# Kernel tuning notes

Measured on AMD Instinct MI355X. Metric: run time of the kernel, lower is better.

The kernel has to match this reference:

```python
import jax, jax.numpy as jnp
import numpy as np

B, S, H, NH, I, V, P, T = 8, 512, 768, 12, 3072, 30522, 512, 2
D = H // NH
EPS = 1e-12


def _ln(x, g, b):
    m = x.mean(-1, keepdims=True)
    v = ((x - m) ** 2).mean(-1, keepdims=True)
    return (x - m) / jnp.sqrt(v + EPS) * g + b


def setup_inputs() -> dict:
    key = jax.random.key(0)
    ks = jax.random.split(key, 24)
    s = 0.02
    f32 = jnp.float32
    d = {
        'x': jax.random.randint(ks[0], (B, S), 0, V, dtype=jnp.int32),
        'W_word': (jax.random.normal(ks[1], (V, H)) * s).astype(f32),
        'W_pos': (jax.random.normal(ks[2], (P, H)) * s).astype(f32),
        'W_type': (jax.random.normal(ks[3], (T, H)) * s).astype(f32),
        'g_emb': jnp.ones((H,), f32), 'b_emb': jnp.zeros((H,), f32),
        'Wq': (jax.random.normal(ks[4], (H, H)) * s).astype(f32), 'bq': jnp.zeros((H,), f32),
        'Wk': (jax.random.normal(ks[5], (H, H)) * s).astype(f32), 'bk': jnp.zeros((H,), f32),
        'Wv': (jax.random.normal(ks[6], (H, H)) * s).astype(f32), 'bv': jnp.zeros((H,), f32),
        'Wo': (jax.random.normal(ks[7], (H, H)) * s).astype(f32), 'bo': jnp.zeros((H,), f32),
        'g_attn': jnp.ones((H,), f32), 'b_attn': jnp.zeros((H,), f32),
        'Wi': (jax.random.normal(ks[8], (H, I)) * s).astype(f32), 'bi': jnp.zeros((I,), f32),
        'Wd': (jax.random.normal(ks[9], (I, H)) * s).astype(f32), 'bd': jnp.zeros((H,), f32),
        'g_out': jnp.ones((H,), f32), 'b_out': jnp.zeros((H,), f32),
        'Wp': (jax.random.normal(ks[10], (H, H)) * s).astype(f32), 'bp': jnp.zeros((H,), f32),
    }
    return d


def _forward(x, W_word, W_pos, W_type, g_emb, b_emb, Wq, bq, Wk, bk, Wv, bv,
             Wo, bo, g_attn, b_attn, Wi, bi, Wd, bd, g_out, b_out, Wp, bp):
    # embeddings: word + position(arange) + token_type(all zeros -> row 0)
    h = W_word[x] + W_pos[jnp.arange(S)][None, :, :] + W_type[0][None, None, :]
    h = _ln(h, g_emb, b_emb)
    scale = 1.0 / jnp.sqrt(jnp.float32(D))
    # NOTE: the torch module shares one set of layer weights across all 6 layers.
    for _ in range(6):
        q = (h @ Wq + bq).reshape(B, S, NH, D).transpose(0, 2, 1, 3)  # bhsd
        k = (h @ Wk + bk).reshape(B, S, NH, D).transpose(0, 2, 1, 3)
        v = (h @ Wv + bv).reshape(B, S, NH, D).transpose(0, 2, 1, 3)
        scores = jnp.einsum('bhqd,bhkd->bhqk', q, k) * scale
        probs = jax.nn.softmax(scores, axis=-1)
        ctx = jnp.einsum('bhqk,bhkd->bhqd', probs, v)
        ctx = ctx.transpose(0, 2, 1, 3).reshape(B, S, H)
        attn = ctx @ Wo + bo
        xa = _ln(h + attn, g_attn, b_attn)
        ff = jax.nn.gelu(xa @ Wi + bi, approximate=False) @ Wd + bd
        h = _ln(xa + ff, g_out, b_out)
    pooled = h[:, 0, :] @ Wp + bp  # no tanh in the original module
    return h, pooled


def reference(x, W_word, W_pos, W_type, g_emb, b_emb, Wq, bq, Wk, bk, Wv, bv,
              Wo, bo, g_attn, b_attn, Wi, bi, Wd, bd, g_out, b_out, Wp, bp):
    return _forward(x, W_word, W_pos, W_type, g_emb, b_emb, Wq, bq, Wk, bk, Wv, bv,
                    Wo, bo, g_attn, b_attn, Wi, bi, Wd, bd, g_out, b_out, Wp, bp)
```

## Files before the change

### kernel.cpp

```cpp
#include <hip/hip_runtime.h>
#include <hip/hip_bf16.h>
#include <math.h>

#define B_  8
#define S_  512
#define H_  768
#define NH_ 12
#define D_  64
#define I_  3072
#define NTOK (B_*S_)
#define LDQ 2304

typedef __attribute__((ext_vector_type(8))) __bf16 bf16x8;
typedef __attribute__((ext_vector_type(8))) unsigned short ushort8;
typedef __attribute__((ext_vector_type(4))) float  f32x4;

__device__ __forceinline__ float gelu_exact(float x) {
    return 0.5f * x * (1.0f + erff(x * 0.70710678118654752440f));
}

__device__ __forceinline__ unsigned short f2bf(float x) {
    __hip_bfloat16 h = __float2bfloat16(x);
    return *reinterpret_cast<unsigned short*>(&h);
}

__device__ __forceinline__ void gload16(const void* g, void* l) {
    __builtin_amdgcn_global_load_lds(
        (const __attribute__((address_space(1))) void*)g,
        (__attribute__((address_space(3))) void*)l,
        16, 0, 0);
}

#define SB0() __builtin_amdgcn_sched_barrier(0)

__global__ void cvtT_kernel(const float* __restrict__ W, __hip_bfloat16* __restrict__ WT,
                            int K, int N) {
    __shared__ float tile[32][33];
    int k0 = blockIdx.y * 32, n0 = blockIdx.x * 32;
    int tx = threadIdx.x & 31, ty = threadIdx.x >> 5;
    #pragma unroll
    for (int i = 0; i < 32; i += 8)
        tile[ty + i][tx] = W[(long)(k0 + ty + i) * N + n0 + tx];
    __syncthreads();
    #pragma unroll
    for (int i = 0; i < 32; i += 8)
        WT[(long)(n0 + ty + i) * K + k0 + tx] = __float2bfloat16(tile[tx][ty + i]);
}

__global__ void embed_ln_kernel(const int* __restrict__ ids,
                                const float* __restrict__ Wword,
                                const float* __restrict__ Wpos,
                                const float* __restrict__ Wtype,
                                const float* __restrict__ g,
                                const float* __restrict__ b,
                                float* __restrict__ out,
                                __hip_bfloat16* __restrict__ outb) {
    int t = blockIdx.x;
    int s = t % S_;
    long id = ids[t];
    int tid = threadIdx.x;
    float vals[3];
    float sum = 0.f, sq = 0.f;
    #pragma unroll
    for (int i = 0; i < 3; ++i) {
        int c = tid + 256 * i;
        float e = Wword[id * H_ + c] + Wpos[(long)s * H_ + c] + Wtype[c];
        vals[i] = e; sum += e; sq += e * e;
    }
    __shared__ float r1[256], r2[256];
    r1[tid] = sum; r2[tid] = sq; __syncthreads();
    for (int st = 128; st > 0; st >>= 1) {
        if (tid < st) { r1[tid] += r1[tid + st]; r2[tid] += r2[tid + st]; }
        __syncthreads();
    }
    float mean = r1[0] * (1.0f / H_);
    float var  = r2[0] * (1.0f / H_) - mean * mean;
    float inv  = rsqrtf(var + 1e-12f);
    #pragma unroll
    for (int i = 0; i < 3; ++i) {
        int c = tid + 256 * i;
        float v = (vals[i] - mean) * inv * g[c] + b[c];
        out[(long)t * H_ + c] = v;
        outb[(long)t * H_ + c] = __float2bfloat16(v);
    }
}

__global__ void add_ln_kernel(const float* __restrict__ a,
                              const float* __restrict__ r,
                              const float* __restrict__ g,
                              const float* __restrict__ bb,
                              float* __restrict__ out,
                              __hip_bfloat16* __restrict__ outb) {
    int t = blockIdx.x;
    int tid = threadIdx.x;
    float vals[3];
    float sum = 0.f, sq = 0.f;
    #pragma unroll
    for (int i = 0; i < 3; ++i) {
        int c = tid + 256 * i;
        float e = a[(long)t * H_ + c] + r[(long)t * H_ + c];
        vals[i] = e; sum += e; sq += e * e;
    }
    __shared__ float r1[256], r2[256];
    r1[tid] = sum; r2[tid] = sq; __syncthreads();
    for (int st = 128; st > 0; st >>= 1) {
        if (tid < st) { r1[tid] += r1[tid + st]; r2[tid] += r2[tid + st]; }
        __syncthreads();
    }
    float mean = r1[0] * (1.0f / H_);
    float var  = r2[0] * (1.0f / H_) - mean * mean;
    float inv  = rsqrtf(var + 1e-12f);
    #pragma unroll
    for (int i = 0; i < 3; ++i) {
        int c = tid + 256 * i;
        float v = (vals[i] - mean) * inv * g[c] + bb[c];
        out[(long)t * H_ + c] = v;
        outb[(long)t * H_ + c] = __float2bfloat16(v);
    }
}

__global__ void add_ln3_kernel(const float* __restrict__ a,
                               const float* __restrict__ r1p,
                               const float* __restrict__ r2p,
                               const float* __restrict__ g,
                               const float* __restrict__ bb,
                               float* __restrict__ out,
                               __hip_bfloat16* __restrict__ outb) {
    int t = blockIdx.x;
    int tid = threadIdx.x;
    float vals[3];
    float sum = 0.f, sq = 0.f;
    #pragma unroll
    for (int i = 0; i < 3; ++i) {
        int c = tid + 256 * i;
        float e = a[(long)t * H_ + c] + r1p[(long)t * H_ + c] + r2p[(long)t * H_ + c];
        vals[i] = e; sum += e; sq += e * e;
    }
    __shared__ float r1[256], r2[256];
    r1[tid] = sum; r2[tid] = sq; __syncthreads();
    for (int st = 128; st > 0; st >>= 1) {
        if (tid < st) { r1[tid] += r1[tid + st]; r2[tid] += r2[tid + st]; }
        __syncthreads();
    }
    float mean = r1[0] * (1.0f / H_);
    float var  = r2[0] * (1.0f / H_) - mean * mean;
    float inv  = rsqrtf(var + 1e-12f);
    #pragma unroll
    for (int i = 0; i < 3; ++i) {
        int c = tid + 256 * i;
        float v = (vals[i] - mean) * inv * g[c] + bb[c];
        out[(long)t * H_ + c] = v;
        outb[(long)t * H_ + c] = __float2bfloat16(v);
    }
}

template<int BM, int BN, int MI, int NJ, int ACT, int WF32, int WB16>
__global__ __launch_bounds__(256, 6) void mfma_gemm_kernel(
    const __hip_bfloat16* __restrict__ A,
    const __hip_bfloat16* __restrict__ BT,
    const float* __restrict__ bias,
    float* __restrict__ Cf,
    __hip_bfloat16* __restrict__ Cb,
    int M, int N, int Kc, int lda, int ldb) {
    constexpr int WC = BN / (NJ * 16);
    constexpr int WR = BM / (MI * 16);
    static_assert(WR * WC == 4, "4 waves");
    constexpr int LA = BM * 4 / 256;
    constexpr int LB = BN * 4 / 256;
    constexpr int L  = LA + LB;
    __shared__ __align__(16) __hip_bfloat16 sA[2][BM * 32];
    __shared__ __align__(16) __hip_bfloat16 sB[2][BN * 32];
    const int tid  = threadIdx.x;
    const int lane = tid & 63;
    const int w    = tid >> 6;
    const int wr   = w / WC, wc = w % WC;
    const int l15  = lane & 15, l4 = lane >> 4;
    const int m0 = blockIdx.y * BM, n0 = blockIdx.x * BN;
    const int koff = blockIdx.z * Kc;
    const int goff = (l15 >> 1) & 3;

    auto stage = [&](int buf, int k0) {
        #pragma unroll
        for (int t = 0; t < LA; ++t) {
            int c = tid + 256 * t;
            int row = c >> 2, gq = c & 3;
            int gsrc = gq ^ ((row >> 1) & 3);
            gload16(A + (long)(m0 + row) * lda + koff + k0 + gsrc * 8, &sA[buf][row * 32 + gq * 8]);
        }
        #pragma unroll
        for (int t = 0; t < LB; ++t) {
            int c = tid + 256 * t;
            int row = c >> 2, gq = c & 3;
            int gsrc = gq ^ ((row >> 1) & 3);
            gload16(BT + (long)(n0 + row) * ldb + koff + k0 + gsrc * 8, &sB[buf][row * 32 + gq * 8]);
        }
    };

    f32x4 acc[MI][NJ] = {};
    const int nk = Kc >> 5;

    stage(0, 0);
    for (int t = 0; t < nk; ++t) {
        const int cur = t & 1;
        if (t + 1 < nk) {
            stage(cur ^ 1, (t + 1) * 32);
            asm volatile("s_waitcnt vmcnt(%0)" :: "i"(L) : "memory");
        } else {
            asm volatile("s_waitcnt vmcnt(0)" ::: "memory");
        }
        SB0(); __builtin_amdgcn_s_barrier(); SB0();

        const int gsw = (l4 ^ goff) * 8;
        bf16x8 af[MI], bf[NJ];
        #pragma unroll
        for (int i = 0; i < MI; ++i)
            af[i] = *reinterpret_cast<const bf16x8*>(&sA[cur][(wr * MI * 16 + i * 16 + l15) * 32 + gsw]);
        #pragma unroll
        for (int j = 0; j < NJ; ++j)
            bf[j] = *reinterpret_cast<const bf16x8*>(&sB[cur][(wc * NJ * 16 + j * 16 + l15) * 32 + gsw]);
        #pragma unroll
        for (int i = 0; i < MI; ++i)
            #pragma unroll
            for (int j = 0; j < NJ; ++j)
                acc[i][j] = __builtin_amdgcn_mfma_f32_16x16x32_bf16(af[i], bf[j], acc[i][j], 0, 0, 0);

        SB0(); __builtin_amdgcn_s_barrier(); SB0();
    }

    float* Cfz = Cf + (size_t)blockIdx.z * M * N;
    const bool addb = (blockIdx.z == 0);
    #pragma unroll
    for (int i = 0; i < MI; ++i) {
        #pragma unroll
        for (int j = 0; j < NJ; ++j) {
            int col = n0 + wc * NJ * 16 + j * 16 + l15;
            float bv = addb ? bias[col] : 0.f;
            #pragma unroll
            for (int r = 0; r < 4; ++r) {
                int row = m0 + wr * MI * 16 + i * 16 + l4 * 4 + r;
                float v = acc[i][j][r] + bv;
                if (ACT == 1) v = gelu_exact(v);
                if (WF32) Cfz[(long)row * N + col] = v;
                if (WB16) Cb[(long)row * N + col] = __float2bfloat16(v);
            }
        }
    }
}

__global__ __launch_bounds__(256, 4) void flash_attn_kernel(
    const __hip_bfloat16* __restrict__ QKV,
    __hip_bfloat16* __restrict__ Ctx) {
    __shared__ __align__(16) unsigned short sK[64 * 72];
    __shared__ __align__(16) unsigned short sVt[64 * 72];
    __shared__ __align__(16) unsigned short sP[4 * 16 * 72];

    const int tid  = threadIdx.x;
    const int lane = tid & 63;
    const int w    = tid >> 6;
    const int l15  = lane & 15, l4 = lane >> 4;
    const int qb = blockIdx.x;
    const int bh = blockIdx.y;
    const int b  = bh / NH_, hd = bh % NH_;
    const long rbase = (long)b * S_ * LDQ;
    const int qoff = hd * D_, koff = H_ + hd * D_, voff = 2 * H_ + hd * D_;

    const int qrow0 = qb * 64 + w * 16;
    bf16x8 af[2];
    #pragma unroll
    for (int ks = 0; ks < 2; ++ks)
        af[ks] = *reinterpret_cast<const bf16x8*>(
            QKV + rbase + (long)(qrow0 + l15) * LDQ + qoff + ks * 32 + l4 * 8);

    f32x4 ctx[4] = {};
    float m_run[4], l_run[4];
    #pragma unroll
    for (int r = 0; r < 4; ++r) { m_run[r] = -1e30f; l_run[r] = 0.f; }

    const int sr = tid >> 2;
    const int sc = (tid & 3) * 16;
    unsigned short* pl = sP + w * (16 * 72);

    for (int kv0 = 0; kv0 < S_; kv0 += 64) {
        const __hip_bfloat16* kg = QKV + rbase + (long)(kv0 + sr) * LDQ + koff + sc;
        const __hip_bfloat16* vg = QKV + rbase + (long)(kv0 + sr) * LDQ + voff + sc;
        ushort8 kv_a = *reinterpret_cast<const ushort8*>(kg);
        ushort8 kv_b = *reinterpret_cast<const ushort8*>(kg + 8);
        ushort8 vv_a = *reinterpret_cast<const ushort8*>(vg);
        ushort8 vv_b = *reinterpret_cast<const ushort8*>(vg + 8);
        __syncthreads();
        *reinterpret_cast<ushort8*>(sK + sr * 72 + sc)     = kv_a;
        *reinterpret_cast<ushort8*>(sK + sr * 72 + sc + 8) = kv_b;
        #pragma unroll
        for (int i = 0; i < 8; ++i) {
            sVt[(sc + i) * 72 + sr]     = vv_a[i];
            sVt[(sc + 8 + i) * 72 + sr] = vv_b[i];
        }
        __syncthreads();

        f32x4 s[4];
        #pragma unroll
        for (int j = 0; j < 4; ++j) {
            s[j] = (f32x4){0.f, 0.f, 0.f, 0.f};
            #pragma unroll
            for (int ks = 0; ks < 2; ++ks) {
                bf16x8 bk = *reinterpret_cast<const bf16x8*>(sK + (j * 16 + l15) * 72 + ks * 32 + l4 * 8);
                s[j] = __builtin_amdgcn_mfma_f32_16x16x32_bf16(af[ks], bk, s[j], 0, 0, 0);
            }
        }
        #pragma unroll
        for (int j = 0; j < 4; ++j) s[j] *= 0.125f;

        #pragma unroll
        for (int r = 0; r < 4; ++r) {
            float mx = fmaxf(fmaxf(s[0][r], s[1][r]), fmaxf(s[2][r], s[3][r]));
            #pragma unroll
            for (int o = 1; o < 16; o <<= 1) mx = fmaxf(mx, __shfl_xor(mx, o));
            float mnew = fmaxf(m_run[r], mx);
            float sum = 0.f;
            #pragma unroll
            for (int j = 0; j < 4; ++j) {
                float p = __expf(s[j][r] - mnew);
                s[j][r] = p; sum += p;
            }
            #pragma unroll
            for (int o = 1; o < 16; o <<= 1) sum += __shfl_xor(sum, o);
            float resc = __expf(m_run[r] - mnew);
            l_run[r] = l_run[r] * resc + sum;
            m_run[r] = mnew;
            #pragma unroll
            for (int j = 0; j < 4; ++j) ctx[j][r] *= resc;
        }

        #pragma unroll
        for (int j = 0; j < 4; ++j)
            #pragma unroll
            for (int r = 0; r < 4; ++r)
                pl[(l4 * 4 + r) * 72 + j * 16 + l15] = f2bf(s[j][r]);

        #pragma unroll
        for (int ks = 0; ks < 2; ++ks) {
            bf16x8 ap = *reinterpret_cast<const bf16x8*>(pl + l15 * 72 + ks * 32 + l4 * 8);
            #pragma unroll
            for (int jd = 0; jd < 4; ++jd) {
                bf16x8 bv = *reinterpret_cast<const bf16x8*>(sVt + (jd * 16 + l15) * 72 + ks * 32 + l4 * 8);
                ctx[jd] = __builtin_amdgcn_mfma_f32_16x16x32_bf16(ap, bv, ctx[jd], 0, 0, 0);
            }
        }
    }

    #pragma unroll
    for (int r = 0; r < 4; ++r) {
        float inv = 1.f / l_run[r];
        long tok = (long)b * S_ + qb * 64 + w * 16 + l4 * 4 + r;
        #pragma unroll
        for (int jd = 0; jd < 4; ++jd)
            Ctx[tok * H_ + hd * D_ + jd * 16 + l15] = __float2bfloat16(ctx[jd][r] * inv);
    }
}

__global__ void pooled_kernel(const float* __restrict__ h,
                              const float* __restrict__ Wp,
                              const float* __restrict__ bp,
                              float* __restrict__ out) {
    int b = blockIdx.y;
    int col = blockIdx.x * 256 + threadIdx.x;
    const float* hb = h + (long)b * S_ * H_;
    float acc = 0.f;
    #pragma unroll 8
    for (int k = 0; k < H_; ++k)
        acc += hb[k] * Wp[(long)k * H_ + col];
    out[(long)b * H_ + col] = acc + bp[col];
}

extern "C" void kernel_launch(void* const* d_in, const int* in_sizes, int n_in,
                              void* d_out, int out_size, void* d_ws, size_t ws_size,
                              hipStream_t stream) {
    const int*   x      = (const int*)  d_in[0];
    const float* W_word = (const float*)d_in[1];
    const float* W_pos  = (const float*)d_in[2];
    const float* W_type = (const float*)d_in[3];
    const float* g_emb  = (const float*)d_in[4];
    const float* b_emb  = (const float*)d_in[5];
    const float* Wq     = (const float*)d_in[6];
    const float* bq     = (const float*)d_in[7];
    const float* Wk     = (const float*)d_in[8];
    const float* bk     = (const float*)d_in[9];
    const float* Wv     = (const float*)d_in[10];
    const float* bv     = (const float*)d_in[11];
    const float* Wo     = (const float*)d_in[12];
    const float* bo     = (const float*)d_in[13];
    const float* g_attn = (const float*)d_in[14];
    const float* b_attn = (const float*)d_in[15];
    const float* Wi     = (const float*)d_in[16];
    const float* bi     = (const float*)d_in[17];
    const float* Wd     = (const float*)d_in[18];
    const float* bd     = (const float*)d_in[19];
    const float* g_out  = (const float*)d_in[20];
    const float* b_out  = (const float*)d_in[21];
    const float* Wp     = (const float*)d_in[22];
    const float* bp     = (const float*)d_in[23];

    const size_t NT = (size_t)NTOK * H_;
    char* base = (char*)d_ws;
    size_t off = 0;
    auto alloc = [&](size_t bytes) -> char* {
        char* p = base + off;
        off += (bytes + 255) & ~(size_t)255;
        return p;
    };
    float* h    = (float*)alloc(NT * 4);
    float* xa   = (float*)alloc(NT * 4);
    float* kb   = (float*)alloc(NT * 4 * 2);
    float* kb2  = kb + NT;
    __hip_bfloat16* h_b   = (__hip_bfloat16*)alloc(NT * 2);
    __hip_bfloat16* xa_b  = (__hip_bfloat16*)alloc(NT * 2);
    __hip_bfloat16* qkv_b = (__hip_bfloat16*)alloc((size_t)NTOK * LDQ * 2);
    __hip_bfloat16* ctx_b = (__hip_bfloat16*)alloc(NT * 2);
    __hip_bfloat16* ff1_b = (__hip_bfloat16*)alloc((size_t)NTOK * I_ * 2);
    __hip_bfloat16* WqkvT = (__hip_bfloat16*)alloc((size_t)LDQ * H_ * 2);
    __hip_bfloat16* WoT = (__hip_bfloat16*)alloc((size_t)H_ * H_ * 2);
    __hip_bfloat16* WiT = (__hip_bfloat16*)alloc((size_t)H_ * I_ * 2);
    __hip_bfloat16* WdT = (__hip_bfloat16*)alloc((size_t)I_ * H_ * 2);
    float* bqkv = (float*)alloc(LDQ * 4);

    cvtT_kernel<<<dim3(H_/32, H_/32), 256, 0, stream>>>(Wq, WqkvT, H_, H_);
    cvtT_kernel<<<dim3(H_/32, H_/32), 256, 0, stream>>>(Wk, WqkvT + (size_t)H_ * H_, H_, H_);
    cvtT_kernel<<<dim3(H_/32, H_/32), 256, 0, stream>>>(Wv, WqkvT + (size_t)2 * H_ * H_, H_, H_);
    cvtT_kernel<<<dim3(H_/32, H_/32), 256, 0, stream>>>(Wo, WoT, H_, H_);
    cvtT_kernel<<<dim3(I_/32, H_/32), 256, 0, stream>>>(Wi, WiT, H_, I_);
    cvtT_kernel<<<dim3(H_/32, I_/32), 256, 0, stream>>>(Wd, WdT, I_, H_);
    hipMemcpyAsync(bqkv,          bq, H_ * 4, hipMemcpyDeviceToDevice, stream);
    hipMemcpyAsync(bqkv + H_,     bk, H_ * 4, hipMemcpyDeviceToDevice, stream);
    hipMemcpyAsync(bqkv + 2 * H_, bv, H_ * 4, hipMemcpyDeviceToDevice, stream);

    embed_ln_kernel<<<NTOK, 256, 0, stream>>>(x, W_word, W_pos, W_type, g_emb, b_emb, h, h_b);

    dim3 gqkv(LDQ/64, NTOK/128);
    dim3 gi(I_/64, NTOK/128);
    dim3 go(H_/64, NTOK/128, 2);
    dim3 gff2(H_/64, NTOK/128, 2);
    for (int layer = 0; layer < 6; ++layer) {
        mfma_gemm_kernel<128,64,4,2,0,0,1><<<gqkv, 256, 0, stream>>>(
            h_b, WqkvT, bqkv, nullptr, qkv_b, NTOK, LDQ, H_, H_, H_);
        flash_attn_kernel<<<dim3(S_/64, B_*NH_), 256, 0, stream>>>(qkv_b, ctx_b);
        mfma_gemm_kernel<128,64,4,2,0,1,0><<<go, 256, 0, stream>>>(
            ctx_b, WoT, bo, kb, nullptr, NTOK, H_, H_/2, H_, H_);
        add_ln3_kernel<<<NTOK, 256, 0, stream>>>(h, kb, kb2, g_attn, b_attn, xa, xa_b);
        mfma_gemm_kernel<128,64,4,2,1,0,1><<<gi, 256, 0, stream>>>(
            xa_b, WiT, bi, nullptr, ff1_b, NTOK, I_, H_, H_, H_);
        mfma_gemm_kernel<128,64,4,2,0,1,0><<<gff2, 256, 0, stream>>>(
            ff1_b, WdT, bd, kb, nullptr, NTOK, H_, I_/2, I_, I_);
        add_ln3_kernel<<<NTOK, 256, 0, stream>>>(xa, kb, kb2, g_out, b_out, h, h_b);
    }

    hipMemcpyAsync(d_out, h, NT * sizeof(float), hipMemcpyDeviceToDevice, stream);
    pooled_kernel<<<dim3(3, 8), 256, 0, stream>>>(h, Wp, bp, (float*)d_out + NT);
}
```

Before: 1.142 ms.

## Vectorize LayerNorm kernels, split FF2 K four ways, fuse output copy and pooler

The LayerNorm kernels now use 192 threads with float4 loads and stores and a wave-shuffle reduction, replacing the 256-thread shared-memory tree. The FF2 GEMM splits K into four partials instead of two, summed by a new add_ln5 kernel. The last layer writes straight into the output buffer, which removes the final device-to-device copy. The three bias memcpys become one concat kernel, and the pooler uses a bf16 transposed Wp with one wave per output column, which rounds Wp to bf16.

After: 1.148 ms. About the same (+0.6%).

```diff
diff --git a/kernel.cpp b/kernel.cpp
--- a/kernel.cpp
+++ b/kernel.cpp
@@ -13,6 +13,7 @@
 
 typedef __attribute__((ext_vector_type(8))) __bf16 bf16x8;
 typedef __attribute__((ext_vector_type(8))) unsigned short ushort8;
+typedef __attribute__((ext_vector_type(4))) unsigned short ushort4v;
 typedef __attribute__((ext_vector_type(4))) float  f32x4;
 
 __device__ __forceinline__ float gelu_exact(float x) {
@@ -45,6 +46,47 @@
     #pragma unroll
     for (int i = 0; i < 32; i += 8)
         WT[(long)(n0 + ty + i) * K + k0 + tx] = __float2bfloat16(tile[tx][ty + i]);
+}
+
+__global__ void bias_concat_kernel(const float* __restrict__ bq,
+                                   const float* __restrict__ bk,
+                                   const float* __restrict__ bv,
+                                   float* __restrict__ bqkv) {
+    int i = blockIdx.x * 256 + threadIdx.x;
+    const float* src = (i < H_) ? bq : (i < 2 * H_) ? bk : bv;
+    bqkv[i] = src[i % H_];
+}
+
+__device__ __forceinline__ void ln_finish(float e0, float e1, float e2, float e3,
+                                          int tid, float* tot1, float* tot2) {
+    float s1 = e0 + e1 + e2 + e3;
+    float s2 = e0 * e0 + e1 * e1 + e2 * e2 + e3 * e3;
+    #pragma unroll
+    for (int o = 32; o > 0; o >>= 1) { s1 += __shfl_xor(s1, o); s2 += __shfl_xor(s2, o); }
+    __shared__ float ws1[3], ws2[3];
+    int wid = tid >> 6;
+    if ((tid & 63) == 0) { ws1[wid] = s1; ws2[wid] = s2; }
+    __syncthreads();
+    *tot1 = ws1[0] + ws1[1] + ws1[2];
+    *tot2 = ws2[0] + ws2[1] + ws2[2];
+}
+
+__device__ __forceinline__ void ln_store(f32x4 e, float mean, float inv,
+                                         const float* __restrict__ g,
+                                         const float* __restrict__ bb,
+                                         float* __restrict__ out,
+                                         __hip_bfloat16* __restrict__ outb,
+                                         long t, int tid) {
+    f32x4 gv = reinterpret_cast<const f32x4*>(g)[tid];
+    f32x4 bv = reinterpret_cast<const f32x4*>(bb)[tid];
+    f32x4 r;
+    #pragma unroll
+    for (int i = 0; i < 4; ++i) r[i] = (e[i] - mean) * inv * gv[i] + bv[i];
+    reinterpret_cast<f32x4*>(out + t * H_)[tid] = r;
+    ushort4v u;
+    #pragma unroll
+    for (int i = 0; i < 4; ++i) u[i] = f2bf(r[i]);
+    reinterpret_cast<ushort4v*>(reinterpret_cast<unsigned short*>(outb) + t * H_)[tid] = u;
 }
 
 __global__ void embed_ln_kernel(const int* __restrict__ ids,
@@ -55,103 +97,68 @@
                                 const float* __restrict__ b,
                                 float* __restrict__ out,
                                 __hip_bfloat16* __restrict__ outb) {
-    int t = blockIdx.x;
-    int s = t % S_;
+    long t = blockIdx.x;
+    int s = (int)(t % S_);
     long id = ids[t];
     int tid = threadIdx.x;
-    float vals[3];
-    float sum = 0.f, sq = 0.f;
-    #pragma unroll
-    for (int i = 0; i < 3; ++i) {
-        int c = tid + 256 * i;
-        float e = Wword[id * H_ + c] + Wpos[(long)s * H_ + c] + Wtype[c];
-        vals[i] = e; sum += e; sq += e * e;
-    }
-    __shared__ float r1[256], r2[256];
-    r1[tid] = sum; r2[tid] = sq; __syncthreads();
-    for (int st = 128; st > 0; st >>= 1) {
-        if (tid < st) { r1[tid] += r1[tid + st]; r2[tid] += r2[tid + st]; }
-        __syncthreads();
-    }
-    float mean = r1[0] * (1.0f / H_);
-    float var  = r2[0] * (1.0f / H_) - mean * mean;
-    float inv  = rsqrtf(var + 1e-12f);
-    #pragma unroll
-    for (int i = 0; i < 3; ++i) {
-        int c = tid + 256 * i;
-        float v = (vals[i] - mean) * inv * g[c] + b[c];
-        out[(long)t * H_ + c] = v;
-        outb[(long)t * H_ + c] = __float2bfloat16(v);
-    }
-}
-
-__global__ void add_ln_kernel(const float* __restrict__ a,
-                              const float* __restrict__ r,
-                              const float* __restrict__ g,
-                              const float* __restrict__ bb,
-                              float* __restrict__ out,
-                              __hip_bfloat16* __restrict__ outb) {
-    int t = blockIdx.x;
-    int tid = threadIdx.x;
-    float vals[3];
-    float sum = 0.f, sq = 0.f;
-    #pragma unroll
-    for (int i = 0; i < 3; ++i) {
-        int c = tid + 256 * i;
-        float e = a[(long)t * H_ + c] + r[(long)t * H_ + c];
-        vals[i] = e; sum += e; sq += e * e;
-    }
-    __shared__ float r1[256], r2[256];
-    r1[tid] = sum; r2[tid] = sq; __syncthreads();
-    for (int st = 128; st > 0; st >>= 1) {
-        if (tid < st) { r1[tid] += r1[tid + st]; r2[tid] += r2[tid + st]; }
-        __syncthreads();
-    }
-    float mean = r1[0] * (1.0f / H_);
-    float var  = r2[0] * (1.0f / H_) - mean * mean;
-    float inv  = rsqrtf(var + 1e-12f);
-    #pragma unroll
-    for (int i = 0; i < 3; ++i) {
-        int c = tid + 256 * i;
-        float v = (vals[i] - mean) * inv * g[c] + bb[c];
-        out[(long)t * H_ + c] = v;
-        outb[(long)t * H_ + c] = __float2bfloat16(v);
-    }
+    f32x4 e = reinterpret_cast<const f32x4*>(Wword + id * H_)[tid];
+    f32x4 p = reinterpret_cast<const f32x4*>(Wpos + (long)s * H_)[tid];
+    f32x4 y = reinterpret_cast<const f32x4*>(Wtype)[tid];
+    #pragma unroll
+    for (int i = 0; i < 4; ++i) e[i] += p[i] + y[i];
+    float tot1, tot2;
+    ln_finish(e[0], e[1], e[2], e[3], tid, &tot1, &tot2);
+    float mean = tot1 * (1.0f / H_);
+    float var  = tot2 * (1.0f / H_) - mean * mean;
+    ln_store(e, mean, rsqrtf(var + 1e-12f), g, b, out, outb, t, tid);
 }
 
 __global__ void add_ln3_kernel(const float* __restrict__ a,
-                               const float* __restrict__ r1p,
-                               const float* __restrict__ r2p,
+                               const float* __restrict__ p0,
+                               const float* __restrict__ p1,
                                const float* __restrict__ g,
                                const float* __restrict__ bb,
                                float* __restrict__ out,
                                __hip_bfloat16* __restrict__ outb) {
-    int t = blockIdx.x;
+    long t = blockIdx.x;
     int tid = threadIdx.x;
-    float vals[3];
-    float sum = 0.f, sq = 0.f;
-    #pragma unroll
-    for (int i = 0; i < 3; ++i) {
-        int c = tid + 256 * i;
-        float e = a[(long)t * H_ + c] + r1p[(long)t * H_ + c] + r2p[(long)t * H_ + c];
-        vals[i] = e; sum += e; sq += e * e;
-    }
-    __shared__ float r1[256], r2[256];
-    r1[tid] = sum; r2[tid] = sq; __syncthreads();
-    for (int st = 128; st > 0; st >>= 1) {
-        if (tid < st) { r1[tid] += r1[tid + st]; r2[tid] += r2[tid + st]; }
-        __syncthreads();
-    }
-    float mean = r1[0] * (1.0f / H_);
-    float var  = r2[0] * (1.0f / H_) - mean * mean;
-    float inv  = rsqrtf(var + 1e-12f);
-    #pragma unroll
-    for (int i = 0; i < 3; ++i) {
-        int c = tid + 256 * i;
-        float v = (vals[i] - mean) * inv * g[c] + bb[c];
-        out[(long)t * H_ + c] = v;
-        outb[(long)t * H_ + c] = __float2bfloat16(v);
-    }
+    long idx = t * (H_ / 4) + tid;
+    f32x4 e = reinterpret_cast<const f32x4*>(a)[idx];
+    f32x4 u = reinterpret_cast<const f32x4*>(p0)[idx];
+    f32x4 v = reinterpret_cast<const f32x4*>(p1)[idx];
+    #pragma unroll
+    for (int i = 0; i < 4; ++i) e[i] += u[i] + v[i];
+    float tot1, tot2;
+    ln_finish(e[0], e[1], e[2], e[3], tid, &tot1, &tot2);
+    float mean = tot1 * (1.0f / H_);
+    float var  = tot2 * (1.0f / H_) - mean * mean;
+    ln_store(e, mean, rsqrtf(var + 1e-12f), g, bb, out, outb, t, tid);
+}
+
+__global__ void add_ln5_kernel(const float* __restrict__ a,
+                               const float* __restrict__ p0,
+                               const float* __restrict__ p1,
+                               const float* __restrict__ p2,
+                               const float* __restrict__ p3,
+                               const float* __restrict__ g,
+                               const float* __restrict__ bb,
+                               float* __restrict__ out,
+                               __hip_bfloat16* __restrict__ outb) {
+    long t = blockIdx.x;
+    int tid = threadIdx.x;
+    long idx = t * (H_ / 4) + tid;
+    f32x4 e  = reinterpret_cast<const f32x4*>(a)[idx];
+    f32x4 u0 = reinterpret_cast<const f32x4*>(p0)[idx];
+    f32x4 u1 = reinterpret_cast<const f32x4*>(p1)[idx];
+    f32x4 u2 = reinterpret_cast<const f32x4*>(p2)[idx];
+    f32x4 u3 = reinterpret_cast<const f32x4*>(p3)[idx];
+    #pragma unroll
+    for (int i = 0; i < 4; ++i) e[i] += u0[i] + u1[i] + u2[i] + u3[i];
+    float tot1, tot2;
+    ln_finish(e[0], e[1], e[2], e[3], tid, &tot1, &tot2);
+    float mean = tot1 * (1.0f / H_);
+    float var  = tot2 * (1.0f / H_) - mean * mean;
+    ln_store(e, mean, rsqrtf(var + 1e-12f), g, bb, out, outb, t, tid);
 }
 
 template<int BM, int BN, int MI, int NJ, int ACT, int WF32, int WB16>
@@ -358,18 +365,23 @@
     }
 }
 
-__global__ void pooled_kernel(const float* __restrict__ h,
-                              const float* __restrict__ Wp,
-                              const float* __restrict__ bp,
-                              float* __restrict__ out) {
-    int b = blockIdx.y;
-    int col = blockIdx.x * 256 + threadIdx.x;
+__global__ void pooled2_kernel(const float* __restrict__ h,
+                               const __hip_bfloat16* __restrict__ WpT,
+                               const float* __restrict__ bp,
+                               float* __restrict__ out) {
+    const int col = blockIdx.x, b = blockIdx.y;
+    const int lane = threadIdx.x;
     const float* hb = h + (long)b * S_ * H_;
+    const __hip_bfloat16* wp = WpT + (long)col * H_;
     float acc = 0.f;
-    #pragma unroll 8
-    for (int k = 0; k < H_; ++k)
-        acc += hb[k] * Wp[(long)k * H_ + col];
-    out[(long)b * H_ + col] = acc + bp[col];
+    #pragma unroll
+    for (int i = 0; i < H_ / 64; ++i) {
+        int k = lane + i * 64;
+        acc += hb[k] * __bfloat162float(wp[k]);
+    }
+    #pragma unroll
+    for (int o = 32; o > 0; o >>= 1) acc += __shfl_xor(acc, o);
+    if (lane == 0) out[(long)b * H_ + col] = acc + bp[col];
 }
 
 extern "C" void kernel_launch(void* const* d_in, const int* in_sizes, int n_in,
@@ -410,8 +422,10 @@
     };
     float* h    = (float*)alloc(NT * 4);
     float* xa   = (float*)alloc(NT * 4);
-    float* kb   = (float*)alloc(NT * 4 * 2);
-    float* kb2  = kb + NT;
+    float* kb   = (float*)alloc(NT * 4 * 4);
+    float* kb1  = kb + NT;
+    float* kb2  = kb + 2 * NT;
+    float* kb3  = kb + 3 * NT;
     __hip_bfloat16* h_b   = (__hip_bfloat16*)alloc(NT * 2);
     __hip_bfloat16* xa_b  = (__hip_bfloat16*)alloc(NT * 2);
     __hip_bfloat16* qkv_b = (__hip_bfloat16*)alloc((size_t)NTOK * LDQ * 2);
@@ -421,6 +435,7 @@
     __hip_bfloat16* WoT = (__hip_bfloat16*)alloc((size_t)H_ * H_ * 2);
     __hip_bfloat16* WiT = (__hip_bfloat16*)alloc((size_t)H_ * I_ * 2);
     __hip_bfloat16* WdT = (__hip_bfloat16*)alloc((size_t)I_ * H_ * 2);
+    __hip_bfloat16* WpT = (__hip_bfloat16*)alloc((size_t)H_ * H_ * 2);
     float* bqkv = (float*)alloc(LDQ * 4);
 
     cvtT_kernel<<<dim3(H_/32, H_/32), 256, 0, stream>>>(Wq, WqkvT, H_, H_);
@@ -429,30 +444,31 @@
     cvtT_kernel<<<dim3(H_/32, H_/32), 256, 0, stream>>>(Wo, WoT, H_, H_);
     cvtT_kernel<<<dim3(I_/32, H_/32), 256, 0, stream>>>(Wi, WiT, H_, I_);
     cvtT_kernel<<<dim3(H_/32, I_/32), 256, 0, stream>>>(Wd, WdT, I_, H_);
-    hipMemcpyAsync(bqkv,          bq, H_ * 4, hipMemcpyDeviceToDevice, stream);
-    hipMemcpyAsync(bqkv + H_,     bk, H_ * 4, hipMemcpyDeviceToDevice, stream);
-    hipMemcpyAsync(bqkv + 2 * H_, bv, H_ * 4, hipMemcpyDeviceToDevice, stream);
-
-    embed_ln_kernel<<<NTOK, 256, 0, stream>>>(x, W_word, W_pos, W_type, g_emb, b_emb, h, h_b);
-
+    cvtT_kernel<<<dim3(H_/32, H_/32), 256, 0, stream>>>(Wp, WpT, H_, H_);
+    bias_concat_kernel<<<LDQ/256, 256, 0, stream>>>(bq, bk, bv, bqkv);
+
+    embed_ln_kernel<<<NTOK, 192, 0, stream>>>(x, W_word, W_pos, W_type, g_emb, b_emb, h, h_b);
+
+    float* hout = (float*)d_out;
     dim3 gqkv(LDQ/64, NTOK/128);
     dim3 gi(I_/64, NTOK/128);
     dim3 go(H_/64, NTOK/128, 2);
-    dim3 gff2(H_/64, NTOK/128, 2);
+    dim3 gff2(H_/64, NTOK/128, 4);
     for (int layer = 0; layer < 6; ++layer) {
         mfma_gemm_kernel<128,64,4,2,0,0,1><<<gqkv, 256, 0, stream>>>(
             h_b, WqkvT, bqkv, nullptr, qkv_b, NTOK, LDQ, H_, H_, H_);
         flash_attn_kernel<<<dim3(S_/64, B_*NH_), 256, 0, stream>>>(qkv_b, ctx_b);
         mfma_gemm_kernel<128,64,4,2,0,1,0><<<go, 256, 0, stream>>>(
             ctx_b, WoT, bo, kb, nullptr, NTOK, H_, H_/2, H_, H_);
-        add_ln3_kernel<<<NTOK, 256, 0, stream>>>(h, kb, kb2, g_attn, b_attn, xa, xa_b);
+        add_ln3_kernel<<<NTOK, 192, 0, stream>>>(h, kb, kb1, g_attn, b_attn, xa, xa_b);
         mfma_gemm_kernel<128,64,4,2,1,0,1><<<gi, 256, 0, stream>>>(
             xa_b, WiT, bi, nullptr, ff1_b, NTOK, I_, H_, H_, H_);
         mfma_gemm_kernel<128,64,4,2,0,1,0><<<gff2, 256, 0, stream>>>(
-            ff1_b, WdT, bd, kb, nullptr, NTOK, H_, I_/2, I_, I_);
-        add_ln3_kernel<<<NTOK, 256, 0, stream>>>(xa, kb, kb2, g_out, b_out, h, h_b);
-    }
-
-    hipMemcpyAsync(d_out, h, NT * sizeof(float), hipMemcpyDeviceToDevice, stream);
-    pooled_kernel<<<dim3(3, 8), 256, 0, stream>>>(h, Wp, bp, (float*)d_out + NT);
-}
+            ff1_b, WdT, bd, kb, nullptr, NTOK, H_, I_/4, I_, I_);
+        float* dst = (layer == 5) ? hout : h;
+        add_ln5_kernel<<<NTOK, 192, 0, stream>>>(xa, kb, kb1, kb2, kb3,
+                                                 g_out, b_out, dst, h_b);
+    }
+
+    pooled2_kernel<<<dim3(H_, B_), 64, 0, stream>>>(hout, WpT, bp, (float*)d_out + NT);
+}
```
